# Kernel optimization log

Hardware: AMD Instinct MI355X
Metric: run time of the kernel (lower is better)

Reference implementation:

```python
import jax, jax.numpy as jnp
import numpy as np

EPS = 1e-8
C_RGLRU = 8.0  # Griffin constant

def rmsnorm(x, w):
    rms = jnp.sqrt(jnp.mean(x * x, axis=-1, keepdims=True) + EPS)
    return w * (x / rms)

def causal_depthwise_conv(x, conv_w, conv_b):
    # x: [B,S,H], conv_w: [K,H] depthwise causal conv, left-padded
    K = conv_w.shape[0]
    S = x.shape[1]
    xp = jnp.pad(x, ((0, 0), (K - 1, 0), (0, 0)))
    y = sum(conv_w[k] * xp[:, k:k + S, :] for k in range(K))
    return y + conv_b

def rg_lru(x, ga_W, ga_b, gx_W, gx_b, a_param):
    # x: [B,S,H]. Griffin RG-LRU: h_t = a_t h_{t-1} + sqrt(1-a_t^2) (i_t * x_t)
    r = jax.nn.sigmoid(x @ ga_W + ga_b)          # recurrence gate
    i = jax.nn.sigmoid(x @ gx_W + gx_b)          # input gate
    log_a = -C_RGLRU * jax.nn.softplus(a_param) * r
    a = jnp.exp(log_a)
    mult = jnp.sqrt(-jnp.expm1(2.0 * log_a))     # sqrt(1 - a^2), stable
    b = mult * (i * x)
    def combine(c1, c2):
        a1, b1 = c1
        a2, b2 = c2
        return a1 * a2, a2 * b1 + b2
    _, h = jax.lax.associative_scan(combine, (a, b), axis=1)
    return h

def setup_inputs() -> dict:
    D, H, F, K, B, S = 2048, 2048, 6144, 4, 2, 2048
    key = jax.random.key(0)
    ks = jax.random.split(key, 16)
    def lin(k, fan_in, shape):
        return jax.random.normal(k, shape, jnp.float32) * (fan_in ** -0.5)
    return {
        "x": jax.random.normal(ks[0], (B, S, D), jnp.float32),
        "norm1_w": jnp.ones((D,), jnp.float32),
        "left_W": lin(ks[1], D, (D, H)), "left_b": jnp.zeros((H,), jnp.float32),
        "right_W": lin(ks[2], D, (D, H)), "right_b": jnp.zeros((H,), jnp.float32),
        "conv_w": lin(ks[3], K, (K, H)), "conv_b": jnp.zeros((H,), jnp.float32),
        "ga_W": lin(ks[4], H, (H, H)), "ga_b": jnp.zeros((H,), jnp.float32),
        "gx_W": lin(ks[5], H, (H, H)), "gx_b": jnp.zeros((H,), jnp.float32),
        "a_param": jax.random.uniform(ks[6], (H,), jnp.float32, 0.5, 3.0),
        "out_W": lin(ks[7], H, (H, D)), "out_b": jnp.zeros((D,), jnp.float32),
        "norm2_w": jnp.ones((D,), jnp.float32),
        "up1_W": lin(ks[8], D, (D, F)), "up1_b": jnp.zeros((F,), jnp.float32),
        "up2_W": lin(ks[9], D, (D, F)), "up2_b": jnp.zeros((F,), jnp.float32),
        "down_W": lin(ks[10], F, (F, D)), "down_b": jnp.zeros((D,), jnp.float32),
    }

def reference(x, norm1_w, left_W, left_b, right_W, right_b, conv_w, conv_b,
              ga_W, ga_b, gx_W, gx_b, a_param, out_W, out_b,
              norm2_w, up1_W, up1_b, up2_W, up2_b, down_W, down_b):
    gelu = lambda t: jax.nn.gelu(t, approximate=False)
    # recurrent sub-block (pre-norm residual)
    xn = rmsnorm(x, norm1_w)
    left = gelu(xn @ left_W + left_b)
    right = rg_lru(causal_depthwise_conv(xn @ right_W + right_b, conv_w, conv_b),
                   ga_W, ga_b, gx_W, gx_b, a_param)
    x1 = (left * right) @ out_W + out_b + x
    # gated MLP sub-block (pre-norm residual)
    x1n = rmsnorm(x1, norm2_w)
    mlp = (gelu(x1n @ up1_W + up1_b) * (x1n @ up2_W + up2_b)) @ down_W + down_b
    return mlp + x1
```

## Files before the change

### kernel.cpp

```cpp
#include <hip/hip_runtime.h>
#include <cstdint>
#include <cstdio>

typedef __bf16 bf16x8 __attribute__((ext_vector_type(8)));
typedef float  f32x4  __attribute__((ext_vector_type(4)));
typedef const __attribute__((address_space(1))) void* gas_ptr;
typedef __attribute__((address_space(3))) void* las_ptr;

__device__ __forceinline__ uint16_t f32_to_bf16_rne(float f){
  uint32_t u = __builtin_bit_cast(uint32_t, f);
  u += 0x7FFFu + ((u >> 16) & 1u);
  return (uint16_t)(u >> 16);
}
__device__ __forceinline__ float bf16_to_f32(uint16_t h){
  uint32_t u = (uint32_t)h << 16;
  return __builtin_bit_cast(float, u);
}
__device__ __forceinline__ float gelu_exact(float x){
  return 0.5f * x * (1.f + erff(x * 0.7071067811865475f));
}

template<int EPI>
__device__ __forceinline__ void epi_store(float v, size_t idx, int row, int col,
    int N, int SPLIT, const float* auxF, const uint16_t* auxB,
    float* Cf, uint16_t* Cb0, uint16_t* Cb1, bool second)
{
  if constexpr (EPI == 1) {
    if (!second) Cb0[(size_t)row * SPLIT + col] = f32_to_bf16_rne(gelu_exact(v));
    else         Cb1[(size_t)row * (N - SPLIT) + (col - SPLIT)] = f32_to_bf16_rne(v);
  }
  if constexpr (EPI == 2) Cb0[idx] = f32_to_bf16_rne(v);
  if constexpr (EPI == 4) Cb0[idx] = f32_to_bf16_rne(v + auxF[idx]);
  if constexpr (EPI == 5) Cf[idx] = v + bf16_to_f32(auxB[idx]);
}

template<int EPI, int BM>
__global__ __launch_bounds__(512)
void gemm8p(const uint16_t* __restrict__ A, const uint16_t* __restrict__ Bt,
            const float* __restrict__ bias0, const float* __restrict__ bias1,
            const float* __restrict__ auxF, const uint16_t* __restrict__ auxB,
            float* __restrict__ Cf, uint16_t* __restrict__ Cb0, uint16_t* __restrict__ Cb1,
            int M, int N, int K, int SPLIT)
{
  constexpr int BN = 256;
  constexpr int M_REP   = BM / 32;
  constexpr int MH      = M_REP / 2;
  constexpr int LOADS_A = BM / 64;
  constexpr int LOADS_B = BN / 64;
  constexpr int LTOT    = LOADS_A + LOADS_B;
  constexpr int ASIZE   = BM * 128;
  constexpr int ABYTES  = 2 * ASIZE;
  constexpr int BSIZE   = BN * 128;
  __shared__ alignas(16) char smem[2 * (BM + BN) * 128];

  const int tid = threadIdx.x, lane = tid & 63, wid = tid >> 6;
  const int wm = wid >> 2, wn = wid & 3;
  const int la = lane & 15, lq = lane >> 4;
  const int n0 = blockIdx.x * BN, m0 = blockIdx.y * BM;

  const int rt = tid >> 3;
  const int gs = (tid & 7) ^ (rt & 7);
  const uint16_t* srcA = A  + (size_t)(m0 + rt) * K + gs * 8;
  const uint16_t* srcB = Bt + (size_t)(n0 + rt) * K + gs * 8;

  const int rowAb = (wm * (BM / 2) + la) * 128;
  const int rowBb = (wn * 64 + la) * 128;
  const int ck0 = ((lq)     ^ (la & 7)) * 16;
  const int ck1 = ((4 + lq) ^ (la & 7)) * 16;

  f32x4 acc[M_REP][4];
  const f32x4 fz = {0.f, 0.f, 0.f, 0.f};
#pragma unroll
  for (int m = 0; m < M_REP; ++m)
#pragma unroll
    for (int n = 0; n < 4; ++n) acc[m][n] = fz;

  bf16x8 aF[MH][2], bF0[2][2], bF1[2][2];
  const int NT = K >> 6;

#define STAGE_A8(KT, BUF) do { _Pragma("unroll")                              \
    for (int l = 0; l < LOADS_A; ++l)                                         \
      __builtin_amdgcn_global_load_lds(                                       \
          (gas_ptr)(srcA + (size_t)(KT) * 64 + (size_t)l * 64 * K),           \
          (las_ptr)(smem + (BUF) * ASIZE + (l * 512 + tid) * 16), 16, 0, 0);  \
  } while (0)
#define STAGE_B8(KT, BUF) do { _Pragma("unroll")                              \
    for (int l = 0; l < LOADS_B; ++l)                                         \
      __builtin_amdgcn_global_load_lds(                                       \
          (gas_ptr)(srcB + (size_t)(KT) * 64 + (size_t)l * 64 * K),           \
          (las_ptr)(smem + ABYTES + (BUF) * BSIZE + (l * 512 + tid) * 16),    \
          16, 0, 0);                                                          \
  } while (0)
#define RD_B8(DST, NH, BUF) do { _Pragma("unroll")                            \
    for (int nq = 0; nq < 2; ++nq) {                                          \
      int ro_ = ABYTES + (BUF) * BSIZE + rowBb + ((NH) * 2 + nq) * 2048;      \
      DST[nq][0] = *(const bf16x8*)(smem + ro_ + ck0);                        \
      DST[nq][1] = *(const bf16x8*)(smem + ro_ + ck1);                        \
    }                                                                         \
  } while (0)
#define RD_A8(MHS, BUF) do { _Pragma("unroll")                                \
    for (int mq = 0; mq < MH; ++mq) {                                         \
      int ro_ = (BUF) * ASIZE + rowAb + ((MHS) * MH + mq) * 2048;             \
      aF[mq][0] = *(const bf16x8*)(smem + ro_ + ck0);                         \
      aF[mq][1] = *(const bf16x8*)(smem + ro_ + ck1);                         \
    }                                                                         \
  } while (0)
#define MM8(MHS, NH, BF) do { _Pragma("unroll")                               \
    for (int mq = 0; mq < MH; ++mq)                                           \
      _Pragma("unroll")                                                       \
      for (int nq = 0; nq < 2; ++nq) {                                        \
        acc[(MHS)*MH+mq][(NH)*2+nq] = __builtin_amdgcn_mfma_f32_16x16x32_bf16(\
            aF[mq][0], BF[nq][0], acc[(MHS)*MH+mq][(NH)*2+nq], 0, 0, 0);      \
        acc[(MHS)*MH+mq][(NH)*2+nq] = __builtin_amdgcn_mfma_f32_16x16x32_bf16(\
            aF[mq][1], BF[nq][1], acc[(MHS)*MH+mq][(NH)*2+nq], 0, 0, 0);      \
      }                                                                       \
  } while (0)
#define BARR() __builtin_amdgcn_s_barrier()

  STAGE_A8(0, 0); STAGE_B8(0, 0);
  STAGE_A8(1, 1); STAGE_B8(1, 1);
  asm volatile("s_waitcnt vmcnt(%0)" :: "i"(LTOT) : "memory");
  BARR();

  for (int t = 0; t < NT; ++t) {
    const int buf = t & 1;
    const bool pf = (t + 2 < NT);
    RD_B8(bF0, 0, buf); RD_A8(0, buf);
    BARR();
    __builtin_amdgcn_s_setprio(1); MM8(0, 0, bF0); __builtin_amdgcn_s_setprio(0);
    BARR();
    RD_B8(bF1, 1, buf);
    BARR();
    __builtin_amdgcn_s_setprio(1); MM8(0, 1, bF1); __builtin_amdgcn_s_setprio(0);
    BARR();
    RD_A8(1, buf);
    if (pf) STAGE_B8(t + 2, buf);
    BARR();
    __builtin_amdgcn_s_setprio(1); MM8(1, 0, bF0); __builtin_amdgcn_s_setprio(0);
    BARR();
    if (pf) STAGE_A8(t + 2, buf);
    BARR();
    __builtin_amdgcn_s_setprio(1); MM8(1, 1, bF1); __builtin_amdgcn_s_setprio(0);
    if (pf) asm volatile("s_waitcnt vmcnt(%0)" :: "i"(LTOT) : "memory");
    else    asm volatile("s_waitcnt vmcnt(0)" ::: "memory");
    BARR();
  }
#undef STAGE_A8
#undef STAGE_B8
#undef RD_B8
#undef RD_A8
#undef MM8
#undef BARR

  if constexpr (EPI == 6) {
    const int GN = N >> 1;
#pragma unroll
    for (int np = 0; np < 2; ++np) {
      int gcol = (n0 >> 1) + wn * 32 + np * 16 + la;
      float b1 = bias0[gcol], b2 = bias1[gcol];
#pragma unroll
      for (int m = 0; m < M_REP; ++m) {
        int rbase = m0 + wm * (BM / 2) + m * 16 + lq * 4;
#pragma unroll
        for (int r = 0; r < 4; ++r) {
          int row = rbase + r;
          float v1 = acc[m][2*np][r] + b1;
          float v2 = acc[m][2*np+1][r] + b2;
          Cb0[(size_t)row * GN + gcol] = f32_to_bf16_rne(gelu_exact(v1) * v2);
        }
      }
    }
  } else {
#pragma unroll
    for (int n = 0; n < 4; ++n) {
      int col = n0 + wn * 64 + n * 16 + la;
      const bool second = (col >= SPLIT);
      float bv = second ? bias1[col - SPLIT] : bias0[col];
#pragma unroll
      for (int m = 0; m < M_REP; ++m) {
        int rbase = m0 + wm * (BM / 2) + m * 16 + lq * 4;
#pragma unroll
        for (int r = 0; r < 4; ++r) {
          int row = rbase + r;
          size_t idx = (size_t)row * N + col;
          epi_store<EPI>(acc[m][n][r] + bv, idx, row, col, N, SPLIT, auxF, auxB, Cf, Cb0, Cb1, second);
        }
      }
    }
  }
}

__global__ __launch_bounds__(256)
void cvt_transpose(const float* __restrict__ in, uint16_t* __restrict__ out, int R, int C)
{
  __shared__ float tile[64][65];
  const int r0 = blockIdx.y * 64, c0 = blockIdx.x * 64;
  const int t = threadIdx.x;
  const int lc = (t & 15) * 4;
  const int lr0 = t >> 4;
#pragma unroll
  for (int j = 0; j < 4; j++){
    int lr = lr0 + j*16;
    float4 v = *(const float4*)(in + (size_t)(r0 + lr) * C + c0 + lc);
    tile[lr][lc+0] = v.x; tile[lr][lc+1] = v.y; tile[lr][lc+2] = v.z; tile[lr][lc+3] = v.w;
  }
  __syncthreads();
  const int oc = t >> 2;
  const int rseg = (t & 3) * 16;
  alignas(16) uint16_t tmp[16];
#pragma unroll
  for (int j = 0; j < 16; j++) tmp[j] = f32_to_bf16_rne(tile[rseg + j][oc]);
  uint4* dst = (uint4*)(out + (size_t)(c0 + oc) * R + r0 + rseg);
  dst[0] = *(const uint4*)(&tmp[0]);
  dst[1] = *(const uint4*)(&tmp[8]);
}

__global__ __launch_bounds__(256)
void cvt_transpose_ileave(const float* __restrict__ in, uint16_t* __restrict__ out,
                          int R, int C, int half)
{
  __shared__ float tile[64][65];
  const int r0 = blockIdx.y * 64, c0 = blockIdx.x * 64;
  const int t = threadIdx.x;
  const int lc = (t & 15) * 4;
  const int lr0 = t >> 4;
#pragma unroll
  for (int j = 0; j < 4; j++){
    int lr = lr0 + j*16;
    float4 v = *(const float4*)(in + (size_t)(r0 + lr) * C + c0 + lc);
    tile[lr][lc+0] = v.x; tile[lr][lc+1] = v.y; tile[lr][lc+2] = v.z; tile[lr][lc+3] = v.w;
  }
  __syncthreads();
  const int oc = t >> 2;
  const int rseg = (t & 3) * 16;
  const int c = c0 + oc;
  const int wrow = ((c >> 4) << 5) + half * 16 + (c & 15);
  alignas(16) uint16_t tmp[16];
#pragma unroll
  for (int j = 0; j < 16; j++) tmp[j] = f32_to_bf16_rne(tile[rseg + j][oc]);
  uint4* dst = (uint4*)(out + (size_t)wrow * R + r0 + rseg);
  dst[0] = *(const uint4*)(&tmp[0]);
  dst[1] = *(const uint4*)(&tmp[8]);
}

__global__ __launch_bounds__(256)
void rmsnorm_kernel(const float* __restrict__ x, const float* __restrict__ w,
                    uint16_t* __restrict__ out, int D)
{
  const int row = blockIdx.x;
  const float* xr = x + (size_t)row * D;
  const int base = threadIdx.x * 8;
  float4 va = *(const float4*)(xr + base);
  float4 vb = *(const float4*)(xr + base + 4);
  float ss = va.x*va.x + va.y*va.y + va.z*va.z + va.w*va.w
           + vb.x*vb.x + vb.y*vb.y + vb.z*vb.z + vb.w*vb.w;
#pragma unroll
  for (int o = 32; o > 0; o >>= 1) ss += __shfl_xor(ss, o);
  __shared__ float red[4];
  if ((threadIdx.x & 63) == 0) red[threadIdx.x >> 6] = ss;
  __syncthreads();
  float tot = red[0] + red[1] + red[2] + red[3];
  float inv = rsqrtf(tot / (float)D + 1e-8f);
  float4 wa = *(const float4*)(w + base);
  float4 wb = *(const float4*)(w + base + 4);
  alignas(16) uint16_t tmp[8];
  tmp[0] = f32_to_bf16_rne(va.x * wa.x * inv);
  tmp[1] = f32_to_bf16_rne(va.y * wa.y * inv);
  tmp[2] = f32_to_bf16_rne(va.z * wa.z * inv);
  tmp[3] = f32_to_bf16_rne(va.w * wa.w * inv);
  tmp[4] = f32_to_bf16_rne(vb.x * wb.x * inv);
  tmp[5] = f32_to_bf16_rne(vb.y * wb.y * inv);
  tmp[6] = f32_to_bf16_rne(vb.z * wb.z * inv);
  tmp[7] = f32_to_bf16_rne(vb.w * wb.w * inv);
  *(uint4*)(out + (size_t)row * D + base) = *(const uint4*)tmp;
}

__global__ __launch_bounds__(256)
void rmsnorm_bf16_kernel(const uint16_t* __restrict__ x, const float* __restrict__ w,
                         uint16_t* __restrict__ out, int D)
{
  const int row = blockIdx.x;
  const uint16_t* xr = x + (size_t)row * D;
  const int base = threadIdx.x * 8;
  uint4 v = *(const uint4*)(xr + base);
  const uint16_t* vp = (const uint16_t*)&v;
  float xs[8];
  float ss = 0.f;
#pragma unroll
  for (int j = 0; j < 8; ++j){ xs[j] = bf16_to_f32(vp[j]); ss += xs[j]*xs[j]; }
#pragma unroll
  for (int o = 32; o > 0; o >>= 1) ss += __shfl_xor(ss, o);
  __shared__ float red[4];
  if ((threadIdx.x & 63) == 0) red[threadIdx.x >> 6] = ss;
  __syncthreads();
  float tot = red[0] + red[1] + red[2] + red[3];
  float inv = rsqrtf(tot / (float)D + 1e-8f);
  float4 wa = *(const float4*)(w + base);
  float4 wb = *(const float4*)(w + base + 4);
  float wv[8] = {wa.x, wa.y, wa.z, wa.w, wb.x, wb.y, wb.z, wb.w};
  alignas(16) uint16_t tmp[8];
#pragma unroll
  for (int j = 0; j < 8; ++j) tmp[j] = f32_to_bf16_rne(xs[j] * wv[j] * inv);
  *(uint4*)(out + (size_t)row * D + base) = *(const uint4*)tmp;
}

__global__ __launch_bounds__(256)
void conv_kernel(const uint16_t* __restrict__ xin, const float* __restrict__ cw,
                 const float* __restrict__ cb, uint16_t* __restrict__ yout,
                 int S, int H)
{
  const int h = blockIdx.x * 256 + threadIdx.x;
  const int b = blockIdx.z;
  const int t0 = blockIdx.y * 128;
  const float w0 = cw[h], w1 = cw[H + h], w2 = cw[2*H + h], w3 = cw[3*H + h];
  const float bias = cb[h];
  const size_t colbase = (size_t)b * S * H + h;
  float xm3 = (t0 >= 3) ? bf16_to_f32(xin[colbase + (size_t)(t0-3)*H]) : 0.f;
  float xm2 = (t0 >= 2) ? bf16_to_f32(xin[colbase + (size_t)(t0-2)*H]) : 0.f;
  float xm1 = (t0 >= 1) ? bf16_to_f32(xin[colbase + (size_t)(t0-1)*H]) : 0.f;
  for (int t = t0; t < t0 + 128; ++t){
    size_t idx = colbase + (size_t)t * H;
    float xt = bf16_to_f32(xin[idx]);
    float y = w0*xm3 + w1*xm2 + w2*xm1 + w3*xt + bias;
    yout[idx] = f32_to_bf16_rne(y);
    xm3 = xm2; xm2 = xm1; xm1 = xt;
  }
}

__device__ __forceinline__ void rglru_ab(float rp, float ip, float xc, float coef,
                                         float& a, float& bb)
{
  float r  = 1.f / (1.f + expf(-rp));
  float la = coef * r;
  a = expf(la);
  float mult = sqrtf(-expm1f(2.f * la));
  float ig = 1.f / (1.f + expf(-ip));
  bb = mult * ig * xc;
}

__global__ __launch_bounds__(256)
void scan_phase1(const uint16_t* __restrict__ gpre, const uint16_t* __restrict__ convb,
                 const float* __restrict__ ap,
                 float* __restrict__ SA, float* __restrict__ SB,
                 int S, int H, int T0, int NC)
{
  const int h = blockIdx.x * 256 + threadIdx.x;
  const int j = blockIdx.y, b = blockIdx.z;
  const float coef = -8.f * log1pf(expf(ap[h]));
  size_t rowb = (size_t)b * S + (size_t)j * T0;
  float A = 1.f, Bc = 0.f;
  for (int t = 0; t < T0; ++t){
    size_t row = rowb + t;
    float rp = bf16_to_f32(gpre[row * 2 * H + h]);
    float ip = bf16_to_f32(gpre[row * 2 * H + H + h]);
    float xc = bf16_to_f32(convb[row * H + h]);
    float a, bb; rglru_ab(rp, ip, xc, coef, a, bb);
    A *= a; Bc = a * Bc + bb;
  }
  size_t o = ((size_t)b * NC + j) * H + h;
  SA[o] = A; SB[o] = Bc;
}

__global__ __launch_bounds__(256)
void scan_phase2(const float* __restrict__ SA, const float* __restrict__ SB,
                 float* __restrict__ SH, int H, int NC)
{
  const int h = blockIdx.x * 256 + threadIdx.x;
  const int b = blockIdx.y;
  float hh = 0.f;
  for (int j = 0; j < NC; ++j){
    size_t o = ((size_t)b * NC + j) * H + h;
    SH[o] = hh;
    hh = SA[o] * hh + SB[o];
  }
}

__global__ __launch_bounds__(256)
void scan_phase3(const uint16_t* __restrict__ gpre, const uint16_t* __restrict__ convb,
                 const float* __restrict__ ap, const float* __restrict__ SH,
                 const uint16_t* __restrict__ left, uint16_t* __restrict__ lr,
                 int S, int H, int T0, int NC)
{
  const int h = blockIdx.x * 256 + threadIdx.x;
  const int j = blockIdx.y, b = blockIdx.z;
  const float coef = -8.f * log1pf(expf(ap[h]));
  float hh = SH[((size_t)b * NC + j) * H + h];
  size_t rowb = (size_t)b * S + (size_t)j * T0;
  for (int t = 0; t < T0; ++t){
    size_t row = rowb + t;
    float rp = bf16_to_f32(gpre[row * 2 * H + h]);
    float ip = bf16_to_f32(gpre[row * 2 * H + H + h]);
    float xc = bf16_to_f32(convb[row * H + h]);
    float a, bb; rglru_ab(rp, ip, xc, coef, a, bb);
    hh = a * hh + bb;
    lr[row * H + h] = f32_to_bf16_rne(bf16_to_f32(left[row * H + h]) * hh);
  }
}

extern "C" void kernel_launch(void* const* d_in, const int* in_sizes, int n_in,
                              void* d_out, int out_size, void* d_ws, size_t ws_size,
                              hipStream_t stream)
{
  const int B = 2, S = 2048, D = 2048, H = 2048, F = 6144;
  const int M = B * S;
  const int NC = 32, T0 = S / NC;

  const float* x       = (const float*)d_in[0];
  const float* norm1_w = (const float*)d_in[1];
  const float* left_W  = (const float*)d_in[2];
  const float* left_b  = (const float*)d_in[3];
  const float* right_W = (const float*)d_in[4];
  const float* right_b = (const float*)d_in[5];
  const float* conv_w  = (const float*)d_in[6];
  const float* conv_b  = (const float*)d_in[7];
  const float* ga_W    = (const float*)d_in[8];
  const float* ga_b    = (const float*)d_in[9];
  const float* gx_W    = (const float*)d_in[10];
  const float* gx_b    = (const float*)d_in[11];
  const float* a_param = (const float*)d_in[12];
  const float* out_W   = (const float*)d_in[13];
  const float* out_b   = (const float*)d_in[14];
  const float* norm2_w = (const float*)d_in[15];
  const float* up1_W   = (const float*)d_in[16];
  const float* up1_b   = (const float*)d_in[17];
  const float* up2_W   = (const float*)d_in[18];
  const float* up2_b   = (const float*)d_in[19];
  const float* down_W  = (const float*)d_in[20];
  const float* down_b  = (const float*)d_in[21];

  char* ws = (char*)d_ws;
  size_t off = 0;
  auto alloc = [&](size_t bytes) -> char* {
    char* p = ws + off; off += (bytes + 255) & ~(size_t)255; return p;
  };
  uint16_t* WT    = (uint16_t*)alloc((size_t)2 * F * D * 2);
  uint16_t* XN    = (uint16_t*)alloc((size_t)M * D * 2);
  uint16_t* LEFT  = (uint16_t*)alloc((size_t)M * H * 2);
  uint16_t* RPRE  = (uint16_t*)alloc((size_t)M * H * 2);
  uint16_t* CONVB = (uint16_t*)alloc((size_t)M * H * 2);
  uint16_t* GPRE  = (uint16_t*)alloc((size_t)M * 2 * H * 2);
  uint16_t* LR    = (uint16_t*)alloc((size_t)M * H * 2);
  uint16_t* X1B   = (uint16_t*)alloc((size_t)M * D * 2);
  uint16_t* X1N   = (uint16_t*)alloc((size_t)M * D * 2);
  float*    SA    = (float*)   alloc((size_t)B * NC * H * 4);
  float*    SB    = (float*)   alloc((size_t)B * NC * H * 4);
  float*    SHB   = (float*)   alloc((size_t)B * NC * H * 4);
  uint16_t* G     = XN;

  if (off > ws_size) {
    fprintf(stderr, "kernel_launch: ws too small, need %zu have %zu\n", off, ws_size);
    return;
  }

  float* OUT = (float*)d_out;
  dim3 blk(256);
  dim3 gblk(512);

  rmsnorm_kernel<<<M, blk, 0, stream>>>(x, norm1_w, XN, D);

  cvt_transpose<<<dim3(H/64, D/64), blk, 0, stream>>>(left_W, WT, D, H);
  cvt_transpose<<<dim3(H/64, D/64), blk, 0, stream>>>(right_W, WT + (size_t)H * D, D, H);
  gemm8p<1, 256><<<dim3((2*H)/256, M/256), gblk, 0, stream>>>(
      XN, WT, left_b, right_b, nullptr, nullptr, nullptr, LEFT, RPRE, M, 2*H, D, H);

  conv_kernel<<<dim3(H/256, S/128, B), blk, 0, stream>>>(RPRE, conv_w, conv_b, CONVB, S, H);

  cvt_transpose<<<dim3(H/64, H/64), blk, 0, stream>>>(ga_W, WT, H, H);
  cvt_transpose<<<dim3(H/64, H/64), blk, 0, stream>>>(gx_W, WT + (size_t)H * H, H, H);
  gemm8p<2, 256><<<dim3((2*H)/256, M/256), gblk, 0, stream>>>(
      CONVB, WT, ga_b, gx_b, nullptr, nullptr, nullptr, GPRE, nullptr, M, 2*H, H, H);

  scan_phase1<<<dim3(H/256, NC, B), blk, 0, stream>>>(GPRE, CONVB, a_param, SA, SB, S, H, T0, NC);
  scan_phase2<<<dim3(H/256, B), blk, 0, stream>>>(SA, SB, SHB, H, NC);
  scan_phase3<<<dim3(H/256, NC, B), blk, 0, stream>>>(GPRE, CONVB, a_param, SHB, LEFT, LR, S, H, T0, NC);

  cvt_transpose<<<dim3(D/64, H/64), blk, 0, stream>>>(out_W, WT, H, D);
  gemm8p<4, 128><<<dim3(D/256, M/128), gblk, 0, stream>>>(
      LR, WT, out_b, out_b, x, nullptr, nullptr, X1B, nullptr, M, D, H, D);

  rmsnorm_bf16_kernel<<<M, blk, 0, stream>>>(X1B, norm2_w, X1N, D);

  cvt_transpose_ileave<<<dim3(F/64, D/64), blk, 0, stream>>>(up1_W, WT, D, F, 0);
  cvt_transpose_ileave<<<dim3(F/64, D/64), blk, 0, stream>>>(up2_W, WT, D, F, 1);
  gemm8p<6, 256><<<dim3((2*F)/256, M/256), gblk, 0, stream>>>(
      X1N, WT, up1_b, up2_b, nullptr, nullptr, nullptr, G, nullptr, M, 2*F, D, 2*F);

  cvt_transpose<<<dim3(D/64, F/64), blk, 0, stream>>>(down_W, WT, F, D);
  gemm8p<5, 128><<<dim3(D/256, M/128), gblk, 0, stream>>>(
      G, WT, down_b, down_b, nullptr, X1B, OUT, nullptr, nullptr, M, D, F, D);
}
```

Before: 747.9 us.

## Add triple-buffered GEMM with async global-to-LDS loads for N=D projections

```diff
diff --git a/kernel.cpp b/kernel.cpp
--- a/kernel.cpp
+++ b/kernel.cpp
@@ -190,6 +190,125 @@
   }
 }
 
+template<int EPI, int BM>
+__global__ __launch_bounds__(512)
+void gemm3b(const uint16_t* __restrict__ A, const uint16_t* __restrict__ Bt,
+            const float* __restrict__ bias0, const float* __restrict__ bias1,
+            const float* __restrict__ auxF, const uint16_t* __restrict__ auxB,
+            float* __restrict__ Cf, uint16_t* __restrict__ Cb0, uint16_t* __restrict__ Cb1,
+            int M, int N, int K, int SPLIT)
+{
+  constexpr int BN = 256;
+  constexpr int M_REP   = BM / 32;
+  constexpr int LOADS_A = BM / 64;
+  constexpr int LOADS_B = BN / 64;
+  constexpr int LTOT    = LOADS_A + LOADS_B;
+  constexpr int BUFB    = (BM + BN) * 128;
+  __shared__ alignas(16) char smem[3 * BUFB];
+
+  const int tid  = threadIdx.x;
+  const int lane = tid & 63;
+  const int wid  = tid >> 6;
+  const int wm = wid >> 2, wn = wid & 3;
+  const int la = lane & 15, lq = lane >> 4;
+  const int n0 = blockIdx.x * BN;
+  const int m0 = blockIdx.y * BM;
+
+  const int rt = tid >> 3;
+  const int gs = (tid & 7) ^ (rt & 7);
+  const uint16_t* srcA = A  + (size_t)(m0 + rt) * K + gs * 8;
+  const uint16_t* srcB = Bt + (size_t)(n0 + rt) * K + gs * 8;
+
+  const int rowAb = (wm * (BM / 2) + la) * 128;
+  const int rowBb = BM * 128 + (wn * 64 + la) * 128;
+  const int ck0 = ((lq)     ^ (la & 7)) * 16;
+  const int ck1 = ((4 + lq) ^ (la & 7)) * 16;
+
+  f32x4 acc[M_REP][4];
+  const f32x4 fz = {0.f, 0.f, 0.f, 0.f};
+#pragma unroll
+  for (int m = 0; m < M_REP; ++m)
+#pragma unroll
+    for (int n = 0; n < 4; ++n) acc[m][n] = fz;
+
+  const int NT = K >> 6;
+
+#define STAGE3(KT, BUF) do {                                                  \
+    const uint16_t* sa_ = srcA + (size_t)(KT) * 64;                           \
+    const uint16_t* sb_ = srcB + (size_t)(KT) * 64;                           \
+    char* base_ = smem + (BUF) * BUFB;                                        \
+    _Pragma("unroll")                                                         \
+    for (int l = 0; l < LOADS_A; ++l)                                         \
+      __builtin_amdgcn_global_load_lds((gas_ptr)(sa_ + (size_t)l * 64 * K),   \
+          (las_ptr)(base_ + (l * 512 + tid) * 16), 16, 0, 0);                 \
+    _Pragma("unroll")                                                         \
+    for (int l = 0; l < LOADS_B; ++l)                                         \
+      __builtin_amdgcn_global_load_lds((gas_ptr)(sb_ + (size_t)l * 64 * K),   \
+          (las_ptr)(base_ + BM * 128 + (l * 512 + tid) * 16), 16, 0, 0);      \
+  } while (0)
+
+  STAGE3(0, 0);
+  STAGE3(1, 1);
+  asm volatile("s_waitcnt vmcnt(%0)" :: "i"(LTOT) : "memory");
+  __builtin_amdgcn_s_barrier();
+
+  int cur = 0;
+  for (int t = 0; t < NT; ++t) {
+    const bool pf = (t + 2 < NT);
+    if (pf) {
+      int nxt = cur + 2; if (nxt >= 3) nxt -= 3;
+      STAGE3(t + 2, nxt);
+    }
+    const char* base = smem + cur * BUFB;
+
+    bf16x8 bF[4][2];
+#pragma unroll
+    for (int n = 0; n < 4; ++n) {
+      const char* ro = base + rowBb + n * 2048;
+      bF[n][0] = *(const bf16x8*)(ro + ck0);
+      bF[n][1] = *(const bf16x8*)(ro + ck1);
+    }
+    __builtin_amdgcn_s_setprio(1);
+#pragma unroll
+    for (int m = 0; m < M_REP; ++m) {
+      const char* ro = base + rowAb + m * 2048;
+      bf16x8 a0 = *(const bf16x8*)(ro + ck0);
+      bf16x8 a1 = *(const bf16x8*)(ro + ck1);
+#pragma unroll
+      for (int n = 0; n < 4; ++n) {
+        acc[m][n] = __builtin_amdgcn_mfma_f32_16x16x32_bf16(a0, bF[n][0], acc[m][n], 0, 0, 0);
+        acc[m][n] = __builtin_amdgcn_mfma_f32_16x16x32_bf16(a1, bF[n][1], acc[m][n], 0, 0, 0);
+      }
+    }
+    __builtin_amdgcn_s_setprio(0);
+
+    if (t + 1 < NT) {
+      if (pf) asm volatile("s_waitcnt vmcnt(%0)" :: "i"(LTOT) : "memory");
+      else    asm volatile("s_waitcnt vmcnt(0)" ::: "memory");
+      __builtin_amdgcn_s_barrier();
+      cur += 1; if (cur >= 3) cur -= 3;
+    }
+  }
+#undef STAGE3
+
+#pragma unroll
+  for (int n = 0; n < 4; ++n) {
+    int col = n0 + wn * 64 + n * 16 + la;
+    const bool second = (col >= SPLIT);
+    float bv = second ? bias1[col - SPLIT] : bias0[col];
+#pragma unroll
+    for (int m = 0; m < M_REP; ++m) {
+      int rbase = m0 + wm * (BM / 2) + m * 16 + lq * 4;
+#pragma unroll
+      for (int r = 0; r < 4; ++r) {
+        int row = rbase + r;
+        size_t idx = (size_t)row * N + col;
+        epi_store<EPI>(acc[m][n][r] + bv, idx, row, col, N, SPLIT, auxF, auxB, Cf, Cb0, Cb1, second);
+      }
+    }
+  }
+}
+
 __global__ __launch_bounds__(256)
 void cvt_transpose(const float* __restrict__ in, uint16_t* __restrict__ out, int R, int C)
 {
@@ -475,7 +594,7 @@
   scan_phase3<<<dim3(H/256, NC, B), blk, 0, stream>>>(GPRE, CONVB, a_param, SHB, LEFT, LR, S, H, T0, NC);
 
   cvt_transpose<<<dim3(D/64, H/64), blk, 0, stream>>>(out_W, WT, H, D);
-  gemm8p<4, 128><<<dim3(D/256, M/128), gblk, 0, stream>>>(
+  gemm3b<4, 128><<<dim3(D/256, M/128), gblk, 0, stream>>>(
       LR, WT, out_b, out_b, x, nullptr, nullptr, X1B, nullptr, M, D, H, D);
 
   rmsnorm_bf16_kernel<<<M, blk, 0, stream>>>(X1B, norm2_w, X1N, D);
@@ -486,6 +605,6 @@
       X1N, WT, up1_b, up2_b, nullptr, nullptr, nullptr, G, nullptr, M, 2*F, D, 2*F);
 
   cvt_transpose<<<dim3(D/64, F/64), blk, 0, stream>>>(down_W, WT, F, D);
-  gemm8p<5, 128><<<dim3(D/256, M/128), gblk, 0, stream>>>(
+  gemm3b<5, 128><<<dim3(D/256, M/128), gblk, 0, stream>>>(
       G, WT, down_b, down_b, nullptr, X1B, OUT, nullptr, nullptr, M, D, F, D);
 }
```

New measurement: 741.2 us. About the same (-0.9%).
